# Optimization experiments

Hardware: AMD Instinct MI355X
Metric: run time of the kernel (lower is better)

Reference implementation:

```python
import jax, jax.numpy as jnp
import numpy as np

D_MODEL = 1024
NUM_HEADS = 16
DEPTH = D_MODEL // NUM_HEADS
B, S = 2, 2048


def setup_inputs() -> dict:
    key = jax.random.key(0)
    k1, k2, k3 = jax.random.split(key, 3)
    x = jax.random.normal(k1, (B, S, D_MODEL), dtype=jnp.float32)
    # causal mask: 1.0 where attention is disallowed (upper triangle)
    causal = 1.0 - jnp.tril(jnp.ones((S, S), dtype=jnp.float32))
    mask = causal[None, None, :, :]  # [1,1,S,S]
    w_attn = jax.random.normal(k2, (D_MODEL, 3 * D_MODEL), dtype=jnp.float32) * 0.02
    b_attn = jnp.zeros((3 * D_MODEL,), dtype=jnp.float32)
    w_proj = jax.random.normal(k3, (D_MODEL, D_MODEL), dtype=jnp.float32) * 0.02
    b_proj = jnp.zeros((D_MODEL,), dtype=jnp.float32)
    return {"x": x, "mask": mask, "w_attn": w_attn, "b_attn": b_attn,
            "w_proj": w_proj, "b_proj": b_proj}


def _split_heads(t):
    # [B,S,D] -> [B,H,S,depth]
    b, s, _ = t.shape
    return t.reshape(b, s, NUM_HEADS, DEPTH).transpose(0, 2, 1, 3)


def reference(x, mask, w_attn, b_attn, w_proj, b_proj):
    # QKV projection (Conv1d == pointwise dense over last axis)
    qkv = jnp.einsum('bsd,de->bse', x, w_attn) + b_attn
    q, k, v = jnp.split(qkv, 3, axis=2)
    q, k, v = _split_heads(q), _split_heads(k), _split_heads(v)  # [B,H,S,depth]
    present = jnp.stack([k, v], axis=1)  # [B,2,H,S,depth]
    # scaled dot-product attention (inference: no dropout)
    scores = jnp.einsum('bhqd,bhkd->bhqk', q, k) / jnp.sqrt(
        jnp.asarray(DEPTH, dtype=x.dtype))
    scores = scores + mask * (-1e9)
    attn = jax.nn.softmax(scores, axis=-1)
    out = jnp.einsum('bhqk,bhkd->bhqd', attn, v)
    # merge heads: [B,H,S,depth] -> [B,S,D]
    out = out.transpose(0, 2, 1, 3).reshape(x.shape[0], -1, D_MODEL)
    out = jnp.einsum('bsd,de->bse', out, w_proj) + b_proj
    return out, present
```

## Files before the change

kernel.cpp:

```cpp
#include <hip/hip_runtime.h>
#include <stdint.h>

typedef unsigned short u16;
typedef unsigned int u32;
typedef short bf16x8 __attribute__((ext_vector_type(8)));
typedef float f32x4 __attribute__((ext_vector_type(4)));
typedef float f32x16 __attribute__((ext_vector_type(16)));

#define SEQ 2048
#define NH 16
#define DM 1024
#define DEPTH 64

#define QSCALE 0.18033688f
#define SMAX 16.0f

__device__ __forceinline__ u16 f2bf(float f) {
  union { float f; u32 i; } v; v.f = f;
  u32 x = v.i;
  x += 0x7fffu + ((x >> 16) & 1u);
  return (u16)(x >> 16);
}

__device__ __forceinline__ float bf2f(u16 b) {
  union { u32 i; float f; } u; u.i = ((u32)b) << 16; return u.f;
}

__device__ __forceinline__ float fexp2(float x) {
#if __has_builtin(__builtin_amdgcn_exp2f)
  return __builtin_amdgcn_exp2f(x);
#else
  return exp2f(x);
#endif
}

__device__ __forceinline__ void gload_lds16(const u16* g, u16* l) {
  __builtin_amdgcn_global_load_lds(
      (const __attribute__((address_space(1))) u32*)g,
      (__attribute__((address_space(3))) u32*)l, 16, 0, 0);
}

__global__ __launch_bounds__(256)
void cvt_bf16(const float* __restrict__ src, u16* __restrict__ dst) {
  int i = (blockIdx.x * 256 + threadIdx.x) * 4;
  float4 v = *(const float4*)(src + i);
  ushort4 o; o.x = f2bf(v.x); o.y = f2bf(v.y); o.z = f2bf(v.z); o.w = f2bf(v.w);
  *(ushort4*)(dst + i) = o;
}

__global__ __launch_bounds__(256)
void cvtT_both(const float* __restrict__ wa, const float* __restrict__ wp,
               u16* __restrict__ dwa, u16* __restrict__ dwp) {
  __shared__ float t[32][33];
  const int tid = threadIdx.x;
  const int bx = blockIdx.x;
  const float* src; u16* dst; int N, n0;
  if (bx < 96) { src = wa; dst = dwa; N = 3 * DM; n0 = bx << 5; }
  else         { src = wp; dst = dwp; N = DM;     n0 = (bx - 96) << 5; }
  const int k0 = blockIdx.y << 5;
  const int K = DM;
  {
    int r = tid >> 3, c4 = (tid & 7) << 2;
    float4 v = *(const float4*)(src + (size_t)(k0 + r) * N + n0 + c4);
    t[r][c4 + 0] = v.x; t[r][c4 + 1] = v.y; t[r][c4 + 2] = v.z; t[r][c4 + 3] = v.w;
  }
  __syncthreads();
  {
    int n = tid >> 3, k4 = (tid & 7) << 2;
    ushort4 o;
    o.x = f2bf(t[k4 + 0][n]); o.y = f2bf(t[k4 + 1][n]);
    o.z = f2bf(t[k4 + 2][n]); o.w = f2bf(t[k4 + 3][n]);
    *(ushort4*)(dst + (size_t)(n0 + n) * K + k0 + k4) = o;
  }
}

__global__ __launch_bounds__(256)
void v_transpose(const float* __restrict__ present, u16* __restrict__ vt) {
  __shared__ float t[64][65];
  const int tid = threadIdx.x;
  const int st = blockIdx.x, bh = blockIdx.y;
  const int b = bh >> 4, h = bh & 15;
  const int s0 = st << 6;
  const float* vsrc = present + (((size_t)((b * 2 + 1) * NH + h)) * SEQ + s0) * DEPTH;
  u16* vdst = vt + ((size_t)(b * NH + h) * DEPTH) * SEQ + s0;
#pragma unroll
  for (int i = 0; i < 4; ++i) {
    int e = tid + (i << 8);
    int r = e >> 4, c = e & 15;
    float4 v = *(const float4*)(vsrc + (size_t)r * DEPTH + (c << 2));
    t[r][(c << 2) + 0] = v.x; t[r][(c << 2) + 1] = v.y;
    t[r][(c << 2) + 2] = v.z; t[r][(c << 2) + 3] = v.w;
  }
  __syncthreads();
#pragma unroll
  for (int i = 0; i < 2; ++i) {
    int e = tid + (i << 8);
    int d = e >> 3, s8 = (e & 7) << 3;
    ushort4 o0, o1;
    o0.x = f2bf(t[s8 + 0][d]); o0.y = f2bf(t[s8 + 1][d]);
    o0.z = f2bf(t[s8 + 2][d]); o0.w = f2bf(t[s8 + 3][d]);
    o1.x = f2bf(t[s8 + 4][d]); o1.y = f2bf(t[s8 + 5][d]);
    o1.z = f2bf(t[s8 + 6][d]); o1.w = f2bf(t[s8 + 7][d]);
    *(ushort4*)(vdst + (size_t)d * SEQ + s8) = o0;
    *(ushort4*)(vdst + (size_t)d * SEQ + s8 + 4) = o1;
  }
}

__global__ __launch_bounds__(256)
void gemm_mfma(const u16* __restrict__ A, const u16* __restrict__ Bt,
               const float* __restrict__ bias, int M, int N, int K, int mode,
               float* __restrict__ outf, u16* __restrict__ qws,
               float* __restrict__ present, u16* __restrict__ kbp)
{
  __shared__ __align__(16) u16 As[128][64];
  __shared__ __align__(16) u16 Bs[128][64];
  const int tid = threadIdx.x;
  const int m0 = blockIdx.y << 7;
  const int n0 = blockIdx.x << 7;
  const int w = tid >> 6, lane = tid & 63;
  const int lane15 = lane & 15, quad = lane >> 4;
  const int wm = (w >> 1) << 6, wn = (w & 1) << 6;

  const int srow = lane >> 3;
  const int sseg = (lane & 7) ^ srow;
  const u16* agbase = A  + (size_t)(m0 + w * 32 + srow) * K + sseg * 8;
  const u16* bgbase = Bt + (size_t)(n0 + w * 32 + srow) * K + sseg * 8;

  const int l7 = lane15 & 7;

  f32x4 acc[4][4] = {};

  for (int k0 = 0; k0 < K; k0 += 64) {
#pragma unroll
    for (int i = 0; i < 4; ++i) {
      gload_lds16(agbase + (size_t)(i * 8) * K + k0, &As[w * 32 + i * 8][0]);
      gload_lds16(bgbase + (size_t)(i * 8) * K + k0, &Bs[w * 32 + i * 8][0]);
    }
    __syncthreads();
#pragma unroll
    for (int ks = 0; ks < 2; ++ks) {
      const int fs = ((ks * 4 + quad) ^ l7) << 3;
      bf16x8 af[4], bfr[4];
#pragma unroll
      for (int tm = 0; tm < 4; ++tm)
        af[tm] = *(const bf16x8*)&As[wm + tm * 16 + lane15][fs];
#pragma unroll
      for (int tn = 0; tn < 4; ++tn)
        bfr[tn] = *(const bf16x8*)&Bs[wn + tn * 16 + lane15][fs];
#pragma unroll
      for (int tm = 0; tm < 4; ++tm)
#pragma unroll
        for (int tn = 0; tn < 4; ++tn)
          acc[tm][tn] = __builtin_amdgcn_mfma_f32_16x16x32_bf16(af[tm], bfr[tn], acc[tm][tn], 0, 0, 0);
    }
    __syncthreads();
  }

#pragma unroll
  for (int tn = 0; tn < 4; ++tn) {
    const int c = n0 + wn + tn * 16 + lane15;
    const float bc = bias[c];
    const int t = c >> 10, cc = c & 1023;
    const int h = cc >> 6, d = cc & 63;
#pragma unroll
    for (int tm = 0; tm < 4; ++tm) {
#pragma unroll
      for (int r = 0; r < 4; ++r) {
        const int m = m0 + wm + tm * 16 + quad * 4 + r;
        const float val = acc[tm][tn][r] + bc;
        if (mode == 1) {
          outf[(size_t)m * N + c] = val;
        } else {
          const int b = m >> 11, s = m & 2047;
          if (t == 0) {
            qws[(((size_t)(b * NH + h) * SEQ) + s) * DEPTH + d] = f2bf(val * QSCALE);
          } else {
            const size_t pidx = (((size_t)((b * 2 + (t - 1)) * NH + h) * SEQ) + s) * DEPTH + d;
            present[pidx] = val;
            if (t == 1)
              kbp[(((size_t)(b * NH + h) * SEQ) + s) * DEPTH + d] = f2bf(val);
          }
        }
      }
    }
  }
}

__global__ __launch_bounds__(256)
void attn_mfma(const u16* __restrict__ qb, const u16* __restrict__ kb,
               const u16* __restrict__ vt, u16* __restrict__ attnb)
{
  __shared__ __align__(16) u16 Ks[2][64][64];
  __shared__ __align__(16) u16 Vs[2][64][64];

  const int tid = threadIdx.x;
  const int w = tid >> 6, lane = tid & 63;
  const int l31 = lane & 31, hi = lane >> 5;
  const int qh = w >> 1, kh = w & 1;
  const int p = blockIdx.x, bh = blockIdx.y;
  const int b = bh >> 4, h = bh & 15;

  const u16* qbh = qb + ((size_t)(b * NH + h) * SEQ) * DEPTH;
  const u16* kbh = kb + ((size_t)(b * NH + h) * SEQ) * DEPTH;
  const u16* vbh = vt + ((size_t)(b * NH + h) * DEPTH) * SEQ;

  const int srr = lane >> 3;
  const int sseg = (lane & 7) ^ srr;
  const int r0 = w * 16 + srr;
  const int r1 = r0 + 8;
  const int kr0 = (r0 & ~12) | ((r0 & 4) << 1) | ((r0 & 8) >> 1);
  const int kr1 = (r1 & ~12) | ((r1 & 4) << 1) | ((r1 & 8) >> 1);

  const int rbase = kh * 32 + l31;
  const int swz = l31 & 7;

#pragma unroll 1
  for (int half = 0; half < 2; ++half) {
    const int tt = half ? (31 - p) : p;
    const int sloc = (tt << 6) + qh * 32 + l31;
    __syncthreads();

    gload_lds16(kbh + (size_t)kr0 * DEPTH + sseg * 8, &Ks[0][w * 16][0]);
    gload_lds16(kbh + (size_t)kr1 * DEPTH + sseg * 8, &Ks[0][w * 16 + 8][0]);
    gload_lds16(vbh + (size_t)r0 * SEQ + sseg * 8, &Vs[0][w * 16][0]);
    gload_lds16(vbh + (size_t)r1 * SEQ + sseg * 8, &Vs[0][w * 16 + 8][0]);

    const u16* qrow = qbh + (size_t)sloc * DEPTH + hi * 8;
    bf16x8 qf0 = *(const bf16x8*)(qrow);
    bf16x8 qf1 = *(const bf16x8*)(qrow + 16);
    bf16x8 qf2 = *(const bf16x8*)(qrow + 32);
    bf16x8 qf3 = *(const bf16x8*)(qrow + 48);

    f32x16 accO0 = {};
    f32x16 accO1 = {};
    float L = 0.f;

    const int nch = tt + 1;
    __syncthreads();
#pragma unroll 1
    for (int ct = 0; ct < nch; ++ct) {
      const int bb = ct & 1;
      if (ct + 1 < nch) {
        const int kn = (ct + 1) << 6;
        gload_lds16(kbh + (size_t)(kn + kr0) * DEPTH + sseg * 8, &Ks[bb ^ 1][w * 16][0]);
        gload_lds16(kbh + (size_t)(kn + kr1) * DEPTH + sseg * 8, &Ks[bb ^ 1][w * 16 + 8][0]);
        gload_lds16(vbh + (size_t)r0 * SEQ + kn + sseg * 8, &Vs[bb ^ 1][w * 16][0]);
        gload_lds16(vbh + (size_t)r1 * SEQ + kn + sseg * 8, &Vs[bb ^ 1][w * 16 + 8][0]);
      }
      const bool atdiag = (ct == tt);
      if (!(atdiag && qh == 0 && kh == 1)) {
        f32x16 sc;
#pragma unroll
        for (int j = 0; j < 16; ++j) sc[j] = -SMAX;
        {
          bf16x8 af0 = *(const bf16x8*)&Ks[bb][rbase][((0 + hi) ^ swz) * 8];
          sc = __builtin_amdgcn_mfma_f32_32x32x16_bf16(af0, qf0, sc, 0, 0, 0);
          bf16x8 af1 = *(const bf16x8*)&Ks[bb][rbase][((2 + hi) ^ swz) * 8];
          sc = __builtin_amdgcn_mfma_f32_32x32x16_bf16(af1, qf1, sc, 0, 0, 0);
          bf16x8 af2 = *(const bf16x8*)&Ks[bb][rbase][((4 + hi) ^ swz) * 8];
          sc = __builtin_amdgcn_mfma_f32_32x32x16_bf16(af2, qf2, sc, 0, 0, 0);
          bf16x8 af3 = *(const bf16x8*)&Ks[bb][rbase][((6 + hi) ^ swz) * 8];
          sc = __builtin_amdgcn_mfma_f32_32x32x16_bf16(af3, qf3, sc, 0, 0, 0);
        }
        const bool dmask = atdiag && (qh == kh);
        u16 pb[16];
#pragma unroll
        for (int j = 0; j < 16; ++j) {
          float e = fexp2(sc[j]);
          if (dmask) {
            const int kg = (ct << 6) + kh * 32 + 16 * (j >> 3) + 8 * hi + (j & 7);
            if (kg > sloc) e = 0.f;
          }
          const u16 pbj = f2bf(e);
          pb[j] = pbj;
          L += bf2f(pbj);
        }
        bf16x8 fr0, fr1;
#pragma unroll
        for (int j = 0; j < 8; ++j) { fr0[j] = (short)pb[j]; fr1[j] = (short)pb[8 + j]; }
#pragma unroll
        for (int s = 0; s < 2; ++s) {
          const bf16x8 bp = s ? fr1 : fr0;
          const int vcol = ((kh * 4 + 2 * s + hi) ^ swz) * 8;
          bf16x8 av0 = *(const bf16x8*)&Vs[bb][l31][vcol];
          accO0 = __builtin_amdgcn_mfma_f32_32x32x16_bf16(av0, bp, accO0, 0, 0, 0);
          bf16x8 av1 = *(const bf16x8*)&Vs[bb][32 + l31][vcol];
          accO1 = __builtin_amdgcn_mfma_f32_32x32x16_bf16(av1, bp, accO1, 0, 0, 0);
        }
      }
      __syncthreads();
    }

    float Lw = L + __shfl_xor(L, 32);
    float* red  = (float*)&Ks[0][0][0];
    float* redL = (float*)&Vs[0][0][0];
    const int base = qh * 2048 + lane * 4;
    if (kh) {
#pragma unroll
      for (int g = 0; g < 4; ++g) {
        float4 v0 = make_float4(accO0[4 * g], accO0[4 * g + 1], accO0[4 * g + 2], accO0[4 * g + 3]);
        *(float4*)&red[base + g * 256] = v0;
        float4 v1 = make_float4(accO1[4 * g], accO1[4 * g + 1], accO1[4 * g + 2], accO1[4 * g + 3]);
        *(float4*)&red[base + 1024 + g * 256] = v1;
      }
      redL[qh * 64 + lane] = Lw;
    }
    __syncthreads();
    if (!kh) {
      const float li = 1.0f / (Lw + redL[qh * 64 + lane]);
      u16* ob = attnb + ((size_t)(b * SEQ + sloc)) * DM + h * DEPTH;
#pragma unroll
      for (int g = 0; g < 4; ++g) {
        float4 p0 = *(const float4*)&red[base + g * 256];
        ushort4 st0;
        st0.x = f2bf((accO0[4 * g + 0] + p0.x) * li);
        st0.y = f2bf((accO0[4 * g + 1] + p0.y) * li);
        st0.z = f2bf((accO0[4 * g + 2] + p0.z) * li);
        st0.w = f2bf((accO0[4 * g + 3] + p0.w) * li);
        *(ushort4*)(ob + 8 * g + 4 * hi) = st0;
        float4 p1 = *(const float4*)&red[base + 1024 + g * 256];
        ushort4 st1;
        st1.x = f2bf((accO1[4 * g + 0] + p1.x) * li);
        st1.y = f2bf((accO1[4 * g + 1] + p1.y) * li);
        st1.z = f2bf((accO1[4 * g + 2] + p1.z) * li);
        st1.w = f2bf((accO1[4 * g + 3] + p1.w) * li);
        *(ushort4*)(ob + 32 + 8 * g + 4 * hi) = st1;
      }
    }
  }
}

extern "C" void kernel_launch(void* const* d_in, const int* in_sizes, int n_in,
                              void* d_out, int out_size, void* d_ws, size_t ws_size,
                              hipStream_t stream) {
  (void)in_sizes; (void)n_in; (void)out_size; (void)ws_size;
  const float* x      = (const float*)d_in[0];
  const float* w_attn = (const float*)d_in[2];
  const float* b_attn = (const float*)d_in[3];
  const float* w_proj = (const float*)d_in[4];
  const float* b_proj = (const float*)d_in[5];

  float* out     = (float*)d_out;
  float* present = out + (size_t)2 * SEQ * DM;

  u16* qws   = (u16*)d_ws;
  u16* kbp   = qws + (size_t)4194304;
  u16* xb    = kbp + (size_t)4194304;
  u16* vtp   = xb;
  u16* wabT  = xb + (size_t)4194304;
  u16* attnb = wabT;
  u16* wpbT  = wabT + (size_t)4194304;

  cvt_bf16<<<4096, 256, 0, stream>>>(x, xb);
  cvtT_both<<<dim3(128, 32), 256, 0, stream>>>(w_attn, w_proj, wabT, wpbT);

  gemm_mfma<<<dim3(24, 32), 256, 0, stream>>>(xb, wabT, b_attn,
                                              2 * SEQ, 3 * DM, DM, 0,
                                              nullptr, qws, present, kbp);
  v_transpose<<<dim3(32, 32), 256, 0, stream>>>(present, vtp);
  attn_mfma<<<dim3(16, 32), 256, 0, stream>>>(qws, kbp, vtp, attnb);
  gemm_mfma<<<dim3(8, 32), 256, 0, stream>>>(attnb, wpbT, b_proj,
                                             2 * SEQ, DM, DM, 1,
                                             out, nullptr, nullptr, nullptr);
}
```

Before: 225.6 us.

## Split paired causal attention tiles into separate blocks and use packed bf16 conversion

The attention kernel previously processed two query tiles per block (p and 31-p) to balance causal work. Each block now handles one query tile, and the grid doubles to 32x32, which is meant to raise parallelism and occupancy (launch bounds now request 4 blocks per SM). The softmax probabilities are converted with the packed v_cvt_pk_bf16_f32 instruction instead of scalar rounding. The diagonal mask test is simplified and address offsets are hoisted out of the loop. The cost is that per-block work is now uneven across the grid, which relies on the hardware scheduler to balance load.

```diff
diff --git a/kernel.cpp b/kernel.cpp
--- a/kernel.cpp
+++ b/kernel.cpp
@@ -20,10 +20,6 @@
   u32 x = v.i;
   x += 0x7fffu + ((x >> 16) & 1u);
   return (u16)(x >> 16);
-}
-
-__device__ __forceinline__ float bf2f(u16 b) {
-  union { u32 i; float f; } u; u.i = ((u32)b) << 16; return u.f;
 }
 
 __device__ __forceinline__ float fexp2(float x) {
@@ -32,6 +28,18 @@
 #else
   return exp2f(x);
 #endif
+}
+
+__device__ __forceinline__ u32 cvtpk(float lo, float hi) {
+  u32 r;
+  asm("v_cvt_pk_bf16_f32 %0, %1, %2" : "=v"(r) : "v"(lo), "v"(hi));
+  return r;
+}
+__device__ __forceinline__ float bflo(u32 w) {
+  union { u32 i; float f; } u; u.i = w << 16; return u.f;
+}
+__device__ __forceinline__ float bfhi(u32 w) {
+  union { u32 i; float f; } u; u.i = w & 0xffff0000u; return u.f;
 }
 
 __device__ __forceinline__ void gload_lds16(const u16* g, u16* l) {
@@ -186,7 +194,7 @@
   }
 }
 
-__global__ __launch_bounds__(256)
+__global__ __launch_bounds__(256, 4)
 void attn_mfma(const u16* __restrict__ qb, const u16* __restrict__ kb,
                const u16* __restrict__ vt, u16* __restrict__ attnb)
 {
@@ -197,7 +205,7 @@
   const int w = tid >> 6, lane = tid & 63;
   const int l31 = lane & 31, hi = lane >> 5;
   const int qh = w >> 1, kh = w & 1;
-  const int p = blockIdx.x, bh = blockIdx.y;
+  const int tt = blockIdx.x, bh = blockIdx.y;
   const int b = bh >> 4, h = bh & 15;
 
   const u16* qbh = qb + ((size_t)(b * NH + h) * SEQ) * DEPTH;
@@ -214,118 +222,142 @@
   const int rbase = kh * 32 + l31;
   const int swz = l31 & 7;
 
+  const int sloc = (tt << 6) + qh * 32 + l31;
+  const int nch = tt + 1;
+
+  const int koff0 = ((0 + hi) ^ swz) << 4;
+  const int koff1 = ((2 + hi) ^ swz) << 4;
+  const int koff2 = ((4 + hi) ^ swz) << 4;
+  const int koff3 = ((6 + hi) ^ swz) << 4;
+  const int voffA = ((kh * 4 + 0 + hi) ^ swz) << 4;
+  const int voffB = ((kh * 4 + 2 + hi) ^ swz) << 4;
+
+  const u16* kgp0 = kbh + (size_t)kr0 * DEPTH + sseg * 8;
+  const u16* kgp1 = kbh + (size_t)kr1 * DEPTH + sseg * 8;
+  const u16* vgp0 = vbh + (size_t)r0 * SEQ + sseg * 8;
+  const u16* vgp1 = vbh + (size_t)r1 * SEQ + sseg * 8;
+
+  gload_lds16(kgp0, &Ks[0][w * 16][0]);
+  gload_lds16(kgp1, &Ks[0][w * 16 + 8][0]);
+  gload_lds16(vgp0, &Vs[0][w * 16][0]);
+  gload_lds16(vgp1, &Vs[0][w * 16 + 8][0]);
+
+  const u16* qrow = qbh + (size_t)sloc * DEPTH + hi * 8;
+  bf16x8 qf0 = *(const bf16x8*)(qrow);
+  bf16x8 qf1 = *(const bf16x8*)(qrow + 16);
+  bf16x8 qf2 = *(const bf16x8*)(qrow + 32);
+  bf16x8 qf3 = *(const bf16x8*)(qrow + 48);
+
+  f32x16 accO0 = {};
+  f32x16 accO1 = {};
+  float L = 0.f;
+
+  __syncthreads();
+
 #pragma unroll 1
-  for (int half = 0; half < 2; ++half) {
-    const int tt = half ? (31 - p) : p;
-    const int sloc = (tt << 6) + qh * 32 + l31;
-    __syncthreads();
-
-    gload_lds16(kbh + (size_t)kr0 * DEPTH + sseg * 8, &Ks[0][w * 16][0]);
-    gload_lds16(kbh + (size_t)kr1 * DEPTH + sseg * 8, &Ks[0][w * 16 + 8][0]);
-    gload_lds16(vbh + (size_t)r0 * SEQ + sseg * 8, &Vs[0][w * 16][0]);
-    gload_lds16(vbh + (size_t)r1 * SEQ + sseg * 8, &Vs[0][w * 16 + 8][0]);
-
-    const u16* qrow = qbh + (size_t)sloc * DEPTH + hi * 8;
-    bf16x8 qf0 = *(const bf16x8*)(qrow);
-    bf16x8 qf1 = *(const bf16x8*)(qrow + 16);
-    bf16x8 qf2 = *(const bf16x8*)(qrow + 32);
-    bf16x8 qf3 = *(const bf16x8*)(qrow + 48);
-
-    f32x16 accO0 = {};
-    f32x16 accO1 = {};
-    float L = 0.f;
-
-    const int nch = tt + 1;
-    __syncthreads();
-#pragma unroll 1
-    for (int ct = 0; ct < nch; ++ct) {
-      const int bb = ct & 1;
-      if (ct + 1 < nch) {
-        const int kn = (ct + 1) << 6;
-        gload_lds16(kbh + (size_t)(kn + kr0) * DEPTH + sseg * 8, &Ks[bb ^ 1][w * 16][0]);
-        gload_lds16(kbh + (size_t)(kn + kr1) * DEPTH + sseg * 8, &Ks[bb ^ 1][w * 16 + 8][0]);
-        gload_lds16(vbh + (size_t)r0 * SEQ + kn + sseg * 8, &Vs[bb ^ 1][w * 16][0]);
-        gload_lds16(vbh + (size_t)r1 * SEQ + kn + sseg * 8, &Vs[bb ^ 1][w * 16 + 8][0]);
+  for (int ct = 0; ct < nch; ++ct) {
+    const int bb = ct & 1;
+    if (ct + 1 < nch) {
+      kgp0 += 64 * DEPTH; kgp1 += 64 * DEPTH;
+      vgp0 += 64; vgp1 += 64;
+      gload_lds16(kgp0, &Ks[bb ^ 1][w * 16][0]);
+      gload_lds16(kgp1, &Ks[bb ^ 1][w * 16 + 8][0]);
+      gload_lds16(vgp0, &Vs[bb ^ 1][w * 16][0]);
+      gload_lds16(vgp1, &Vs[bb ^ 1][w * 16 + 8][0]);
+    }
+    const bool atdiag = (ct == tt);
+    if (!(atdiag && qh == 0 && kh == 1)) {
+      const char* kbase = (const char*)&Ks[bb][rbase][0];
+      f32x16 sc;
+#pragma unroll
+      for (int j = 0; j < 16; ++j) sc[j] = -SMAX;
+      {
+        bf16x8 af0 = *(const bf16x8*)(kbase + koff0);
+        sc = __builtin_amdgcn_mfma_f32_32x32x16_bf16(af0, qf0, sc, 0, 0, 0);
+        bf16x8 af1 = *(const bf16x8*)(kbase + koff1);
+        sc = __builtin_amdgcn_mfma_f32_32x32x16_bf16(af1, qf1, sc, 0, 0, 0);
+        bf16x8 af2 = *(const bf16x8*)(kbase + koff2);
+        sc = __builtin_amdgcn_mfma_f32_32x32x16_bf16(af2, qf2, sc, 0, 0, 0);
+        bf16x8 af3 = *(const bf16x8*)(kbase + koff3);
+        sc = __builtin_amdgcn_mfma_f32_32x32x16_bf16(af3, qf3, sc, 0, 0, 0);
       }
-      const bool atdiag = (ct == tt);
-      if (!(atdiag && qh == 0 && kh == 1)) {
-        f32x16 sc;
-#pragma unroll
-        for (int j = 0; j < 16; ++j) sc[j] = -SMAX;
-        {
-          bf16x8 af0 = *(const bf16x8*)&Ks[bb][rbase][((0 + hi) ^ swz) * 8];
-          sc = __builtin_amdgcn_mfma_f32_32x32x16_bf16(af0, qf0, sc, 0, 0, 0);
-          bf16x8 af1 = *(const bf16x8*)&Ks[bb][rbase][((2 + hi) ^ swz) * 8];
-          sc = __builtin_amdgcn_mfma_f32_32x32x16_bf16(af1, qf1, sc, 0, 0, 0);
-          bf16x8 af2 = *(const bf16x8*)&Ks[bb][rbase][((4 + hi) ^ swz) * 8];
-          sc = __builtin_amdgcn_mfma_f32_32x32x16_bf16(af2, qf2, sc, 0, 0, 0);
-          bf16x8 af3 = *(const bf16x8*)&Ks[bb][rbase][((6 + hi) ^ swz) * 8];
-          sc = __builtin_amdgcn_mfma_f32_32x32x16_bf16(af3, qf3, sc, 0, 0, 0);
-        }
-        const bool dmask = atdiag && (qh == kh);
-        u16 pb[16];
+      float pe[16];
+      if (atdiag && (qh == kh)) {
 #pragma unroll
         for (int j = 0; j < 16; ++j) {
           float e = fexp2(sc[j]);
-          if (dmask) {
-            const int kg = (ct << 6) + kh * 32 + 16 * (j >> 3) + 8 * hi + (j & 7);
-            if (kg > sloc) e = 0.f;
-          }
-          const u16 pbj = f2bf(e);
-          pb[j] = pbj;
-          L += bf2f(pbj);
+          if ((16 * (j >> 3) + 8 * hi + (j & 7)) > l31) e = 0.f;
+          pe[j] = e;
         }
-        bf16x8 fr0, fr1;
-#pragma unroll
-        for (int j = 0; j < 8; ++j) { fr0[j] = (short)pb[j]; fr1[j] = (short)pb[8 + j]; }
-#pragma unroll
-        for (int s = 0; s < 2; ++s) {
-          const bf16x8 bp = s ? fr1 : fr0;
-          const int vcol = ((kh * 4 + 2 * s + hi) ^ swz) * 8;
-          bf16x8 av0 = *(const bf16x8*)&Vs[bb][l31][vcol];
-          accO0 = __builtin_amdgcn_mfma_f32_32x32x16_bf16(av0, bp, accO0, 0, 0, 0);
-          bf16x8 av1 = *(const bf16x8*)&Vs[bb][32 + l31][vcol];
-          accO1 = __builtin_amdgcn_mfma_f32_32x32x16_bf16(av1, bp, accO1, 0, 0, 0);
-        }
+      } else {
+#pragma unroll
+        for (int j = 0; j < 16; ++j) pe[j] = fexp2(sc[j]);
       }
-      __syncthreads();
-    }
-
-    float Lw = L + __shfl_xor(L, 32);
-    float* red  = (float*)&Ks[0][0][0];
-    float* redL = (float*)&Vs[0][0][0];
-    const int base = qh * 2048 + lane * 4;
-    if (kh) {
-#pragma unroll
-      for (int g = 0; g < 4; ++g) {
-        float4 v0 = make_float4(accO0[4 * g], accO0[4 * g + 1], accO0[4 * g + 2], accO0[4 * g + 3]);
-        *(float4*)&red[base + g * 256] = v0;
-        float4 v1 = make_float4(accO1[4 * g], accO1[4 * g + 1], accO1[4 * g + 2], accO1[4 * g + 3]);
-        *(float4*)&red[base + 1024 + g * 256] = v1;
+      const u32 pk0 = cvtpk(pe[0], pe[1]),   pk1 = cvtpk(pe[2], pe[3]);
+      const u32 pk2 = cvtpk(pe[4], pe[5]),   pk3 = cvtpk(pe[6], pe[7]);
+      const u32 pk4 = cvtpk(pe[8], pe[9]),   pk5 = cvtpk(pe[10], pe[11]);
+      const u32 pk6 = cvtpk(pe[12], pe[13]), pk7 = cvtpk(pe[14], pe[15]);
+      float l0 = bflo(pk0) + bfhi(pk0);
+      float l1 = bflo(pk1) + bfhi(pk1);
+      l0 += bflo(pk2) + bfhi(pk2);
+      l1 += bflo(pk3) + bfhi(pk3);
+      l0 += bflo(pk4) + bfhi(pk4);
+      l1 += bflo(pk5) + bfhi(pk5);
+      l0 += bflo(pk6) + bfhi(pk6);
+      l1 += bflo(pk7) + bfhi(pk7);
+      L += l0 + l1;
+      union { u32 u[4]; bf16x8 v; } f0, f1;
+      f0.u[0] = pk0; f0.u[1] = pk1; f0.u[2] = pk2; f0.u[3] = pk3;
+      f1.u[0] = pk4; f1.u[1] = pk5; f1.u[2] = pk6; f1.u[3] = pk7;
+      const char* vbase = (const char*)&Vs[bb][l31][0];
+      {
+        bf16x8 av0 = *(const bf16x8*)(vbase + voffA);
+        accO0 = __builtin_amdgcn_mfma_f32_32x32x16_bf16(av0, f0.v, accO0, 0, 0, 0);
+        bf16x8 av1 = *(const bf16x8*)(vbase + 4096 + voffA);
+        accO1 = __builtin_amdgcn_mfma_f32_32x32x16_bf16(av1, f0.v, accO1, 0, 0, 0);
+        bf16x8 av2 = *(const bf16x8*)(vbase + voffB);
+        accO0 = __builtin_amdgcn_mfma_f32_32x32x16_bf16(av2, f1.v, accO0, 0, 0, 0);
+        bf16x8 av3 = *(const bf16x8*)(vbase + 4096 + voffB);
+        accO1 = __builtin_amdgcn_mfma_f32_32x32x16_bf16(av3, f1.v, accO1, 0, 0, 0);
       }
-      redL[qh * 64 + lane] = Lw;
     }
     __syncthreads();
-    if (!kh) {
-      const float li = 1.0f / (Lw + redL[qh * 64 + lane]);
-      u16* ob = attnb + ((size_t)(b * SEQ + sloc)) * DM + h * DEPTH;
-#pragma unroll
-      for (int g = 0; g < 4; ++g) {
-        float4 p0 = *(const float4*)&red[base + g * 256];
-        ushort4 st0;
-        st0.x = f2bf((accO0[4 * g + 0] + p0.x) * li);
-        st0.y = f2bf((accO0[4 * g + 1] + p0.y) * li);
-        st0.z = f2bf((accO0[4 * g + 2] + p0.z) * li);
-        st0.w = f2bf((accO0[4 * g + 3] + p0.w) * li);
-        *(ushort4*)(ob + 8 * g + 4 * hi) = st0;
-        float4 p1 = *(const float4*)&red[base + 1024 + g * 256];
-        ushort4 st1;
-        st1.x = f2bf((accO1[4 * g + 0] + p1.x) * li);
-        st1.y = f2bf((accO1[4 * g + 1] + p1.y) * li);
-        st1.z = f2bf((accO1[4 * g + 2] + p1.z) * li);
-        st1.w = f2bf((accO1[4 * g + 3] + p1.w) * li);
-        *(ushort4*)(ob + 32 + 8 * g + 4 * hi) = st1;
-      }
+  }
+
+  float Lw = L + __shfl_xor(L, 32);
+  float* red  = (float*)&Ks[0][0][0];
+  float* redL = (float*)&Vs[0][0][0];
+  const int base = qh * 2048 + lane * 4;
+  if (kh) {
+#pragma unroll
+    for (int g = 0; g < 4; ++g) {
+      float4 v0 = make_float4(accO0[4 * g], accO0[4 * g + 1], accO0[4 * g + 2], accO0[4 * g + 3]);
+      *(float4*)&red[base + g * 256] = v0;
+      float4 v1 = make_float4(accO1[4 * g], accO1[4 * g + 1], accO1[4 * g + 2], accO1[4 * g + 3]);
+      *(float4*)&red[base + 1024 + g * 256] = v1;
+    }
+    redL[qh * 64 + lane] = Lw;
+  }
+  __syncthreads();
+  if (!kh) {
+    const float li = 1.0f / (Lw + redL[qh * 64 + lane]);
+    u16* ob = attnb + ((size_t)(b * SEQ + sloc)) * DM + h * DEPTH;
+#pragma unroll
+    for (int g = 0; g < 4; ++g) {
+      float4 p0 = *(const float4*)&red[base + g * 256];
+      ushort4 st0;
+      st0.x = f2bf((accO0[4 * g + 0] + p0.x) * li);
+      st0.y = f2bf((accO0[4 * g + 1] + p0.y) * li);
+      st0.z = f2bf((accO0[4 * g + 2] + p0.z) * li);
+      st0.w = f2bf((accO0[4 * g + 3] + p0.w) * li);
+      *(ushort4*)(ob + 8 * g + 4 * hi) = st0;
+      float4 p1 = *(const float4*)&red[base + 1024 + g * 256];
+      ushort4 st1;
+      st1.x = f2bf((accO1[4 * g + 0] + p1.x) * li);
+      st1.y = f2bf((accO1[4 * g + 1] + p1.y) * li);
+      st1.z = f2bf((accO1[4 * g + 2] + p1.z) * li);
+      st1.w = f2bf((accO1[4 * g + 3] + p1.w) * li);
+      *(ushort4*)(ob + 32 + 8 * g + 4 * hi) = st1;
     }
   }
 }
@@ -358,7 +390,7 @@
                                               2 * SEQ, 3 * DM, DM, 0,
                                               nullptr, qws, present, kbp);
   v_transpose<<<dim3(32, 32), 256, 0, stream>>>(present, vtp);
-  attn_mfma<<<dim3(16, 32), 256, 0, stream>>>(qws, kbp, vtp, attnb);
+  attn_mfma<<<dim3(32, 32), 256, 0, stream>>>(qws, kbp, vtp, attnb);
   gemm_mfma<<<dim3(8, 32), 256, 0, stream>>>(attnb, wpbT, b_proj,
                                              2 * SEQ, DM, DM, 1,
                                              out, nullptr, nullptr, nullptr);
```

After: 218.4 us. 3.2% less time.
